# Performance work log

Hardware: AMD Instinct MI355X
Metric: run time of the kernel (lower is better)

## Reference

```python
import jax, jax.numpy as jnp
import numpy as np

DROPOUT_P = 0.5

def _gcn_conv(h, W, b, src, dst, norm, self_norm, n):
    # h: [N, Din] -> [N, Dout]; symmetric-normalized aggregation with self loops
    h = h @ W
    msg = h[src] * norm[:, None]                       # [E, Dout]
    agg = jax.ops.segment_sum(msg, dst, num_segments=n)
    return agg + h * self_norm[:, None] + b


def setup_inputs() -> dict:
    key = jax.random.key(0)
    ks = jax.random.split(key, 8)
    N, E, D_IN, D_OUT = 50000, 800000, 512, 256
    H = 2 * D_OUT  # 512
    x = jax.random.normal(ks[0], (N, D_IN), dtype=jnp.float32)
    edge_index = jax.random.randint(ks[1], (2, E), 0, N, dtype=jnp.int64)
    s = 1.0 / np.sqrt(D_IN)
    W1 = jax.random.uniform(ks[2], (D_IN, H), jnp.float32, -s, s)
    b1 = jnp.zeros((H,), jnp.float32)
    s2 = 1.0 / np.sqrt(H)
    Wmu = jax.random.uniform(ks[3], (H, D_OUT), jnp.float32, -s2, s2)
    bmu = jnp.zeros((D_OUT,), jnp.float32)
    Wls = jax.random.uniform(ks[4], (H, D_OUT), jnp.float32, -s2, s2)
    bls = jnp.zeros((D_OUT,), jnp.float32)
    return {"x": x, "edge_index": edge_index, "W1": W1, "b1": b1,
            "Wmu": Wmu, "bmu": bmu, "Wls": Wls, "bls": bls}


def reference(x, edge_index, W1, b1, Wmu, bmu, Wls, bls):
    n = x.shape[0]
    src, dst = edge_index[0], edge_index[1]
    # GCN symmetric normalization with self loops: deg includes +1 self loop
    deg = jax.ops.segment_sum(jnp.ones_like(dst, dtype=x.dtype), dst, num_segments=n) + 1.0
    dinv = jax.lax.rsqrt(deg)
    norm = dinv[src] * dinv[dst]     # per-edge norm
    self_norm = dinv * dinv          # self-loop norm = 1/deg
    # dropout (train mode, deterministic mask)
    keep = jax.random.bernoulli(jax.random.key(42), 1.0 - DROPOUT_P, x.shape)
    h = jnp.where(keep, x / (1.0 - DROPOUT_P), 0.0)
    h = jax.nn.relu(_gcn_conv(h, W1, b1, src, dst, norm, self_norm, n))
    mu = _gcn_conv(h, Wmu, bmu, src, dst, norm, self_norm, n)
    logstd = _gcn_conv(h, Wls, bls, src, dst, norm, self_norm, n)
    return (mu, logstd)
```

## Files before the change

### kernel.cpp

```cpp
#include <hip/hip_runtime.h>
#include <hip/hip_bf16.h>

typedef __hip_bfloat16 bf16;
typedef __attribute__((ext_vector_type(8))) short short8;
typedef __attribute__((ext_vector_type(4))) float f32x4;

__device__ __forceinline__ float bfu(unsigned short b) {
    unsigned u = ((unsigned)b) << 16;
    float f;
    __builtin_memcpy(&f, &u, 4);
    return f;
}
__device__ __forceinline__ unsigned short f2b(float f) {
    return (unsigned short)(__hip_bfloat16_raw(__float2bfloat16(f)).x);
}

__device__ __forceinline__ void gl_lds16(const void* g, void* l) {
    __builtin_amdgcn_global_load_lds(
        (const __attribute__((address_space(1))) void*)g,
        (__attribute__((address_space(3))) void*)l, 16, 0, 0);
}

__device__ __forceinline__ bool keep_elem(unsigned idx) {
    const unsigned k0 = 0u, k1 = 42u;
    const unsigned k2 = k0 ^ k1 ^ 0x1BD11BDAu;
    unsigned x0 = k0;
    unsigned x1 = idx + k1;
#define TF_QR(R) { x0 += x1; x1 = (x1 << R) | (x1 >> (32 - R)); x1 ^= x0; }
    TF_QR(13) TF_QR(15) TF_QR(26) TF_QR(6)
    x0 += k1; x1 += k2 + 1u;
    TF_QR(17) TF_QR(29) TF_QR(16) TF_QR(24)
    x0 += k2; x1 += k0 + 2u;
    TF_QR(13) TF_QR(15) TF_QR(26) TF_QR(6)
    x0 += k0; x1 += k1 + 3u;
    TF_QR(17) TF_QR(29) TF_QR(16) TF_QR(24)
    x0 += k1; x1 += k2 + 4u;
    TF_QR(13) TF_QR(15) TF_QR(26) TF_QR(6)
    x0 += k2; x1 += k0 + 5u;
#undef TF_QR
    return (((x0 ^ x1) >> 31) & 1u) == 0u;
}

__global__ void detect_edges_k(const unsigned* __restrict__ w, int* __restrict__ flag) {
    __shared__ unsigned red[256];
    unsigned v = 0;
    for (int i = threadIdx.x; i < 2048; i += 256) v |= w[2 * i + 1];
    red[threadIdx.x] = v;
    __syncthreads();
    for (int s = 128; s > 0; s >>= 1) {
        if (threadIdx.x < s) red[threadIdx.x] |= red[threadIdx.x + s];
        __syncthreads();
    }
    if (threadIdx.x == 0) flag[0] = (red[0] == 0u) ? 1 : 0;
}

__global__ void detect_f32_k(const unsigned short* __restrict__ w,
                             int* __restrict__ flag, int fidx) {
    __shared__ int red[256];
    int cnt = 0;
    for (int i = threadIdx.x; i < 1024; i += 256) {
        unsigned short b = w[2 * i];
        int e = (b >> 7) & 0xFF;
        if ((b & 0x7FFF) == 0 || (e >= 100 && e < 140)) cnt++;
    }
    red[threadIdx.x] = cnt;
    __syncthreads();
    for (int s = 128; s > 0; s >>= 1) {
        if (threadIdx.x < s) red[threadIdx.x] += red[threadIdx.x + s];
        __syncthreads();
    }
    if (threadIdx.x == 0) flag[fidx] = (red[0] < 614) ? 1 : 0;
}

__global__ void convert_edges_k(const void* __restrict__ src, int* __restrict__ out,
                                int twoE, const int* __restrict__ flag) {
    int i = blockIdx.x * 256 + threadIdx.x;
    if (i >= twoE) return;
    if (flag[0]) out[i] = (int)((const unsigned long long*)src)[i];
    else         out[i] = ((const int*)src)[i];
}

__global__ void canon_x_drop_k(const void* __restrict__ src, bf16* __restrict__ dst,
                               int n8, const int* __restrict__ flag) {
    int i = blockIdx.x * 256 + threadIdx.x;
    if (i >= n8) return;
    float v[8];
    if (flag[1]) {
        const f32x4* p = (const f32x4*)src;
        f32x4 a = p[2 * i], b = p[2 * i + 1];
#pragma unroll
        for (int k = 0; k < 4; ++k) { v[k] = a[k]; v[4 + k] = b[k]; }
    } else {
        short8 u = ((const short8*)src)[i];
#pragma unroll
        for (int k = 0; k < 8; ++k) v[k] = bfu((unsigned short)u[k]);
    }
    unsigned base = (unsigned)i * 8u;
    short8 o;
#pragma unroll
    for (int k = 0; k < 8; ++k) {
        float f = keep_elem(base + k) ? v[k] * 2.0f : 0.0f;
        o[k] = (short)f2b(f);
    }
    ((short8*)dst)[i] = o;
}

__global__ void canon_k(const void* __restrict__ src, bf16* __restrict__ dst,
                        int n, const int* __restrict__ flag, int fidx) {
    int i = blockIdx.x * 256 + threadIdx.x;
    if (i >= n) return;
    if (flag[fidx]) dst[i] = __float2bfloat16(((const float*)src)[i]);
    else            dst[i] = ((const bf16*)src)[i];
}

__global__ void canon_transpose_k(const void* __restrict__ src, unsigned short* __restrict__ dst,
                                  int K, int Nn, const int* __restrict__ flag, int fidx) {
    __shared__ unsigned short tile[16][17];
    int k0 = blockIdx.x * 16, n0 = blockIdx.y * 16;
    int k = k0 + threadIdx.y, n = n0 + threadIdx.x;
    unsigned short v;
    if (flag[fidx]) v = f2b(((const float*)src)[(size_t)k * Nn + n]);
    else            v = ((const unsigned short*)src)[(size_t)k * Nn + n];
    tile[threadIdx.y][threadIdx.x] = v;
    __syncthreads();
    int nn = n0 + threadIdx.y, kk = k0 + threadIdx.x;
    dst[(size_t)nn * K + kk] = tile[threadIdx.x][threadIdx.y];
}

__global__ void zero_int_k(int* __restrict__ p, int n) {
    int i = blockIdx.x * 256 + threadIdx.x;
    if (i < n) p[i] = 0;
}
__global__ void deg_count_k(const int* __restrict__ edges, int* __restrict__ degi,
                            int E, int n) {
    int e = blockIdx.x * 256 + threadIdx.x;
    if (e >= E) return;
    int d = edges[E + e];
    d = (d < 0) ? 0 : (d >= n ? n - 1 : d);
    atomicAdd(&degi[d], 1);
}
__global__ void dinv_k(const int* __restrict__ degi, float* __restrict__ dinv, int n) {
    int i = blockIdx.x * 256 + threadIdx.x;
    if (i < n) dinv[i] = rsqrtf(1.0f + (float)degi[i]);
}
__global__ void block_sums_k(const int* __restrict__ deg, int* __restrict__ partial, int n) {
    __shared__ int sh[256];
    int i = blockIdx.x * 256 + threadIdx.x;
    sh[threadIdx.x] = (i < n) ? deg[i] : 0;
    __syncthreads();
    for (int s = 128; s > 0; s >>= 1) {
        if (threadIdx.x < s) sh[threadIdx.x] += sh[threadIdx.x + s];
        __syncthreads();
    }
    if (threadIdx.x == 0) partial[blockIdx.x] = sh[0];
}
__global__ void scan_partials_k(int* __restrict__ partial, int G) {
    __shared__ int sh[256];
    int v = (threadIdx.x < G) ? partial[threadIdx.x] : 0;
    sh[threadIdx.x] = v;
    __syncthreads();
    for (int s = 1; s < 256; s <<= 1) {
        int t = 0;
        if (threadIdx.x >= s) t = sh[threadIdx.x - s];
        __syncthreads();
        sh[threadIdx.x] += t;
        __syncthreads();
    }
    if (threadIdx.x < G) partial[threadIdx.x] = sh[threadIdx.x] - v;
}
__global__ void scan_block_k(const int* __restrict__ deg, const int* __restrict__ partial,
                             int* __restrict__ row_ptr, int n) {
    __shared__ int sh[256];
    int i = blockIdx.x * 256 + threadIdx.x;
    int v = (i < n) ? deg[i] : 0;
    sh[threadIdx.x] = v;
    __syncthreads();
    for (int s = 1; s < 256; s <<= 1) {
        int t = 0;
        if (threadIdx.x >= s) t = sh[threadIdx.x - s];
        __syncthreads();
        sh[threadIdx.x] += t;
        __syncthreads();
    }
    int incl = sh[threadIdx.x];
    int base = partial[blockIdx.x];
    if (i < n) row_ptr[i] = base + incl - v;
    if (i == n - 1) row_ptr[n] = base + incl;
}
__global__ void fill_k(const int* __restrict__ edges, const int* __restrict__ row_ptr,
                       int* __restrict__ cnt, int* __restrict__ col, int E, int n) {
    int e = blockIdx.x * 256 + threadIdx.x;
    if (e >= E) return;
    int s = edges[e], d = edges[E + e];
    s = (s < 0) ? 0 : (s >= n ? n - 1 : s);
    d = (d < 0) ? 0 : (d >= n ? n - 1 : d);
    int pos = row_ptr[d] + atomicAdd(&cnt[d], 1);
    col[pos] = s;
}

__global__ __launch_bounds__(256) void gemm_mfma_k(
    const bf16* __restrict__ A, const bf16* __restrict__ Bt,
    bf16* __restrict__ Cb, float* __restrict__ Cf, float* __restrict__ Cf2,
    const bf16* __restrict__ bias, int M, int Nn, int K, int split) {
    __shared__ short sA[128 * 32];
    __shared__ short sB[128 * 32];
    const int tid = threadIdx.x;
    const int lane = tid & 63;
    const int w = tid >> 6;
    const int m0 = blockIdx.x * 128;
    const int n0 = blockIdx.y * 128;
    const int wm = (w >> 1) * 64;
    const int wn = (w & 1) * 64;

    f32x4 acc[4][4] = {};

    const int srow = lane >> 2;
    const int scol = (lane & 3) * 8;

    for (int kk = 0; kk < K; kk += 32) {
#pragma unroll
        for (int q = 0; q < 2; ++q) {
            int r = q * 64 + w * 16 + srow;
            int grow = m0 + r; if (grow >= M) grow = M - 1;
            gl_lds16(A + (size_t)grow * K + kk + scol, &sA[q * 2048 + w * 512 + lane * 8]);
        }
#pragma unroll
        for (int q = 0; q < 2; ++q) {
            int r = q * 64 + w * 16 + srow;
            gl_lds16(Bt + (size_t)(n0 + r) * K + kk + scol, &sB[q * 2048 + w * 512 + lane * 8]);
        }
        __syncthreads();

        const int fr = lane & 15;
        const int fk = (lane >> 4) * 8;
        short8 af[4], bfr[4];
#pragma unroll
        for (int i = 0; i < 4; ++i)
            af[i] = *(const short8*)&sA[(wm + i * 16 + fr) * 32 + fk];
#pragma unroll
        for (int j = 0; j < 4; ++j)
            bfr[j] = *(const short8*)&sB[(wn + j * 16 + fr) * 32 + fk];
#pragma unroll
        for (int i = 0; i < 4; ++i)
#pragma unroll
            for (int j = 0; j < 4; ++j)
                acc[i][j] = __builtin_amdgcn_mfma_f32_16x16x32_bf16(
                    af[i], bfr[j], acc[i][j], 0, 0, 0);
        __syncthreads();
    }

    const int crow = (lane >> 4) * 4;
    const int ccol = lane & 15;
    float* fbase = Cf;
    int nb = n0 + wn;
    int stride = Nn;
    if (Cf2) {
        stride = split;
        if (nb >= split) { fbase = Cf2; nb -= split; }
    }
#pragma unroll
    for (int i = 0; i < 4; ++i) {
#pragma unroll
        for (int r = 0; r < 4; ++r) {
            int row = m0 + wm + i * 16 + crow + r;
            if (row >= M) continue;
            if (Cf) {
                float* cp = fbase + (size_t)row * stride + nb;
#pragma unroll
                for (int j = 0; j < 4; ++j) {
                    int c = j * 16 + ccol;
                    cp[c] = acc[i][j][r] + __bfloat162float(bias[n0 + wn + c]);
                }
            } else {
                bf16* cp = Cb + (size_t)row * Nn + n0 + wn;
#pragma unroll
                for (int j = 0; j < 4; ++j)
                    cp[j * 16 + ccol] = __float2bfloat16(acc[i][j][r]);
            }
        }
    }
}

__global__ __launch_bounds__(256) void gather_k(
    const bf16* __restrict__ t, const int* __restrict__ row_ptr,
    const int* __restrict__ col, const float* __restrict__ dinv,
    const bf16* __restrict__ bias, bf16* __restrict__ outp, int mode, int N) {
    const int node = blockIdx.x * 4 + (threadIdx.x >> 6);
    if (node >= N) return;
    const int lane = threadIdx.x & 63;
    const short8* tp = (const short8*)t;
    const int beg = row_ptr[node];
    const int end = row_ptr[node + 1];
    const float dv = dinv[node];
    float acc[8] = {0.f, 0.f, 0.f, 0.f, 0.f, 0.f, 0.f, 0.f};

    int e = beg;
    const int elim = beg + ((end - beg) & ~7);
    if (e < elim) {
        int c[8];
        float w[8];
#pragma unroll
        for (int k = 0; k < 8; ++k) c[k] = col[e + k];
#pragma unroll
        for (int k = 0; k < 8; ++k) w[k] = dinv[c[k]] * dv;
        for (;;) {
            short8 u[8];
#pragma unroll
            for (int k = 0; k < 8; ++k) u[k] = tp[(size_t)c[k] * 64 + lane];
            const int en = e + 8;
            const bool more = en < elim;
            int cn[8];
            float wn2[8];
            if (more) {
#pragma unroll
                for (int k = 0; k < 8; ++k) cn[k] = col[en + k];
#pragma unroll
                for (int k = 0; k < 8; ++k) wn2[k] = dinv[cn[k]] * dv;
            }
#pragma unroll
            for (int k = 0; k < 8; ++k) {
                const float wk = w[k];
#pragma unroll
                for (int j = 0; j < 8; ++j)
                    acc[j] += wk * bfu((unsigned short)u[k][j]);
            }
            e = en;
            if (!more) break;
#pragma unroll
            for (int k = 0; k < 8; ++k) { c[k] = cn[k]; w[k] = wn2[k]; }
        }
    }
    for (; e + 4 <= end; e += 4) {
        int s0 = col[e + 0], s1 = col[e + 1], s2 = col[e + 2], s3 = col[e + 3];
        float w0 = dinv[s0] * dv, w1 = dinv[s1] * dv;
        float w2 = dinv[s2] * dv, w3 = dinv[s3] * dv;
        short8 u0 = tp[(size_t)s0 * 64 + lane];
        short8 u1 = tp[(size_t)s1 * 64 + lane];
        short8 u2 = tp[(size_t)s2 * 64 + lane];
        short8 u3 = tp[(size_t)s3 * 64 + lane];
#pragma unroll
        for (int k = 0; k < 8; ++k) {
            acc[k] += w0 * bfu((unsigned short)u0[k]);
            acc[k] += w1 * bfu((unsigned short)u1[k]);
            acc[k] += w2 * bfu((unsigned short)u2[k]);
            acc[k] += w3 * bfu((unsigned short)u3[k]);
        }
    }
    for (; e < end; ++e) {
        int s = col[e];
        float w = dinv[s] * dv;
        short8 u = tp[(size_t)s * 64 + lane];
#pragma unroll
        for (int k = 0; k < 8; ++k) acc[k] += w * bfu((unsigned short)u[k]);
    }
    {
        short8 u = tp[(size_t)node * 64 + lane];
        float w = dv * dv;
#pragma unroll
        for (int k = 0; k < 8; ++k) acc[k] += w * bfu((unsigned short)u[k]);
    }
    if (mode == 1) {
        short8 bs = ((const short8*)bias)[lane];
#pragma unroll
        for (int k = 0; k < 8; ++k) {
            acc[k] += bfu((unsigned short)bs[k]);
            acc[k] = fmaxf(acc[k], 0.f);
        }
    }
    short8 o;
#pragma unroll
    for (int k = 0; k < 8; ++k) o[k] = (short)f2b(acc[k]);
    ((short8*)outp)[(size_t)node * 64 + lane] = o;
}

extern "C" void kernel_launch(void* const* d_in, const int* in_sizes, int n_in,
                              void* d_out, int out_size, void* d_ws, size_t ws_size,
                              hipStream_t stream) {
    const void* xin   = d_in[0];
    const void* ei    = d_in[1];
    const void* W1in  = d_in[2];
    const void* b1in  = d_in[3];
    const void* Wmuin = d_in[4];
    const void* bmuin = d_in[5];
    const void* Wlsin = d_in[6];
    const void* blsin = d_in[7];
    float* out = (float*)d_out;

    const int H    = in_sizes[3];
    const int DOUT = in_sizes[5];
    const int DIN  = in_sizes[2] / H;
    const int N    = in_sizes[0] / DIN;
    const int E    = in_sizes[1] / 2;
    const int G    = (N + 255) / 256;

    char* ws = (char*)d_ws;
    size_t off = 0;
    auto alloc = [&](size_t bytes) {
        void* p = ws + off;
        off = (off + bytes + 255) & ~(size_t)255;
        return p;
    };
    int*   flag    = (int*)alloc(256);
    int*   edges   = (int*)alloc((size_t)2 * E * 4);
    int*   degi    = (int*)alloc((size_t)N * 4);
    int*   row_ptr = (int*)alloc((size_t)(N + 1) * 4);
    int*   cnt     = (int*)alloc((size_t)N * 4);
    int*   partial = (int*)alloc((size_t)G * 4);
    int*   col     = (int*)alloc((size_t)E * 4);
    float* dinv    = (float*)alloc((size_t)N * 4);
    bf16*  t1      = (bf16*)alloc((size_t)N * H * 2);
    bf16*  g1      = (bf16*)alloc((size_t)N * H * 2);
    bf16*  xdrop   = (bf16*)alloc((size_t)N * DIN * 2);
    bf16*  W1t     = (bf16*)alloc((size_t)DIN * H * 2);
    bf16*  Wcat    = (bf16*)alloc((size_t)H * 2 * DOUT * 2);
    bf16*  b1c     = (bf16*)alloc((size_t)H * 2);
    bf16*  bcat    = (bf16*)alloc((size_t)2 * DOUT * 2);
    if (off > ws_size) return;

    const int twoE = 2 * E;
    hipLaunchKernelGGL(detect_edges_k, dim3(1), dim3(256), 0, stream, (const unsigned*)ei, flag);
    hipLaunchKernelGGL(detect_f32_k, dim3(1), dim3(256), 0, stream, (const unsigned short*)xin, flag, 1);
    hipLaunchKernelGGL(detect_f32_k, dim3(1), dim3(256), 0, stream, (const unsigned short*)W1in, flag, 2);

    hipLaunchKernelGGL(convert_edges_k, dim3((twoE + 255) / 256), dim3(256), 0, stream,
                       ei, edges, twoE, flag);
    int n8 = (N * DIN) / 8;
    hipLaunchKernelGGL(canon_x_drop_k, dim3((n8 + 255) / 256), dim3(256), 0, stream,
                       xin, xdrop, n8, flag);
    hipLaunchKernelGGL(canon_transpose_k, dim3(DIN / 16, H / 16), dim3(16, 16), 0, stream,
                       W1in, (unsigned short*)W1t, DIN, H, flag, 2);
    hipLaunchKernelGGL(canon_transpose_k, dim3(H / 16, DOUT / 16), dim3(16, 16), 0, stream,
                       Wmuin, (unsigned short*)Wcat, H, DOUT, flag, 2);
    hipLaunchKernelGGL(canon_transpose_k, dim3(H / 16, DOUT / 16), dim3(16, 16), 0, stream,
                       Wlsin, (unsigned short*)(Wcat + (size_t)DOUT * H), H, DOUT, flag, 2);
    hipLaunchKernelGGL(canon_k, dim3(2), dim3(256), 0, stream, b1in, b1c, H, flag, 2);
    hipLaunchKernelGGL(canon_k, dim3(1), dim3(256), 0, stream, bmuin, bcat, DOUT, flag, 2);
    hipLaunchKernelGGL(canon_k, dim3(1), dim3(256), 0, stream, blsin, bcat + DOUT, DOUT, flag, 2);

    hipLaunchKernelGGL(zero_int_k, dim3(G), dim3(256), 0, stream, degi, N);
    hipLaunchKernelGGL(zero_int_k, dim3(G), dim3(256), 0, stream, cnt, N);
    hipLaunchKernelGGL(deg_count_k, dim3((E + 255) / 256), dim3(256), 0, stream, edges, degi, E, N);
    hipLaunchKernelGGL(dinv_k, dim3(G), dim3(256), 0, stream, degi, dinv, N);
    hipLaunchKernelGGL(block_sums_k, dim3(G), dim3(256), 0, stream, degi, partial, N);
    hipLaunchKernelGGL(scan_partials_k, dim3(1), dim3(256), 0, stream, partial, G);
    hipLaunchKernelGGL(scan_block_k, dim3(G), dim3(256), 0, stream, degi, partial, row_ptr, N);
    hipLaunchKernelGGL(fill_k, dim3((E + 255) / 256), dim3(256), 0, stream, edges, row_ptr, cnt, col, E, N);

    hipLaunchKernelGGL(gemm_mfma_k, dim3((N + 127) / 128, H / 128), dim3(256), 0, stream,
                       xdrop, W1t, t1, (float*)nullptr, (float*)nullptr,
                       (const bf16*)nullptr, N, H, DIN, 0);
    bf16* h1 = xdrop;
    hipLaunchKernelGGL(gather_k, dim3((N + 3) / 4), dim3(256), 0, stream,
                       t1, row_ptr, col, dinv, b1c, h1, 1, N);

    hipLaunchKernelGGL(gather_k, dim3((N + 3) / 4), dim3(256), 0, stream,
                       h1, row_ptr, col, dinv, (const bf16*)nullptr, g1, 0, N);
    hipLaunchKernelGGL(gemm_mfma_k, dim3((N + 127) / 128, (2 * DOUT) / 128), dim3(256), 0, stream,
                       g1, Wcat, (bf16*)nullptr, out, out + (size_t)N * DOUT,
                       bcat, N, 2 * DOUT, H, DOUT);
}
```

Before: 659.1 us.

## Fuse dropout into GEMM A-load, widen GEMM tile to full N, merge small kernels

The dropout-and-convert pass over x moves inside the first GEMM's A-tile load, so the bf16 xdrop buffer is never written and read back. The GEMM becomes a 512-thread kernel that covers all 512 output columns per 128-row block, so each A tile is loaded once instead of four times. Flag detection, bias conversion, counter zeroing and dinv are merged into fewer launches. In exchange the Philox-style mask is recomputed in the GEMM's load path with no double buffering, LDS use grows, and occupancy may drop.

```diff
diff --git a/kernel.cpp b/kernel.cpp
--- a/kernel.cpp
+++ b/kernel.cpp
@@ -41,35 +41,37 @@
     return (((x0 ^ x1) >> 31) & 1u) == 0u;
 }
 
-__global__ void detect_edges_k(const unsigned* __restrict__ w, int* __restrict__ flag) {
-    __shared__ unsigned red[256];
-    unsigned v = 0;
-    for (int i = threadIdx.x; i < 2048; i += 256) v |= w[2 * i + 1];
-    red[threadIdx.x] = v;
-    __syncthreads();
-    for (int s = 128; s > 0; s >>= 1) {
-        if (threadIdx.x < s) red[threadIdx.x] |= red[threadIdx.x + s];
-        __syncthreads();
-    }
-    if (threadIdx.x == 0) flag[0] = (red[0] == 0u) ? 1 : 0;
-}
-
-__global__ void detect_f32_k(const unsigned short* __restrict__ w,
-                             int* __restrict__ flag, int fidx) {
+__global__ void detect_all_k(const unsigned* __restrict__ ei,
+                             const unsigned short* __restrict__ x,
+                             const unsigned short* __restrict__ w1,
+                             int* __restrict__ flag) {
     __shared__ int red[256];
-    int cnt = 0;
-    for (int i = threadIdx.x; i < 1024; i += 256) {
-        unsigned short b = w[2 * i];
-        int e = (b >> 7) & 0xFF;
-        if ((b & 0x7FFF) == 0 || (e >= 100 && e < 140)) cnt++;
-    }
-    red[threadIdx.x] = cnt;
-    __syncthreads();
-    for (int s = 128; s > 0; s >>= 1) {
-        if (threadIdx.x < s) red[threadIdx.x] += red[threadIdx.x + s];
-        __syncthreads();
-    }
-    if (threadIdx.x == 0) flag[fidx] = (red[0] < 614) ? 1 : 0;
+    if (blockIdx.x == 0) {
+        unsigned v = 0;
+        for (int i = threadIdx.x; i < 2048; i += 256) v |= ei[2 * i + 1];
+        red[threadIdx.x] = (int)v;
+        __syncthreads();
+        for (int s = 128; s > 0; s >>= 1) {
+            if (threadIdx.x < s) red[threadIdx.x] |= red[threadIdx.x + s];
+            __syncthreads();
+        }
+        if (threadIdx.x == 0) flag[0] = (red[0] == 0) ? 1 : 0;
+    } else {
+        const unsigned short* p = (blockIdx.x == 1) ? x : w1;
+        int cnt = 0;
+        for (int i = threadIdx.x; i < 1024; i += 256) {
+            unsigned short b = p[2 * i];
+            int e = (b >> 7) & 0xFF;
+            if ((b & 0x7FFF) == 0 || (e >= 100 && e < 140)) cnt++;
+        }
+        red[threadIdx.x] = cnt;
+        __syncthreads();
+        for (int s = 128; s > 0; s >>= 1) {
+            if (threadIdx.x < s) red[threadIdx.x] += red[threadIdx.x + s];
+            __syncthreads();
+        }
+        if (threadIdx.x == 0) flag[blockIdx.x] = (red[0] < 614) ? 1 : 0;
+    }
 }
 
 __global__ void convert_edges_k(const void* __restrict__ src, int* __restrict__ out,
@@ -78,39 +80,6 @@
     if (i >= twoE) return;
     if (flag[0]) out[i] = (int)((const unsigned long long*)src)[i];
     else         out[i] = ((const int*)src)[i];
-}
-
-__global__ void canon_x_drop_k(const void* __restrict__ src, bf16* __restrict__ dst,
-                               int n8, const int* __restrict__ flag) {
-    int i = blockIdx.x * 256 + threadIdx.x;
-    if (i >= n8) return;
-    float v[8];
-    if (flag[1]) {
-        const f32x4* p = (const f32x4*)src;
-        f32x4 a = p[2 * i], b = p[2 * i + 1];
-#pragma unroll
-        for (int k = 0; k < 4; ++k) { v[k] = a[k]; v[4 + k] = b[k]; }
-    } else {
-        short8 u = ((const short8*)src)[i];
-#pragma unroll
-        for (int k = 0; k < 8; ++k) v[k] = bfu((unsigned short)u[k]);
-    }
-    unsigned base = (unsigned)i * 8u;
-    short8 o;
-#pragma unroll
-    for (int k = 0; k < 8; ++k) {
-        float f = keep_elem(base + k) ? v[k] * 2.0f : 0.0f;
-        o[k] = (short)f2b(f);
-    }
-    ((short8*)dst)[i] = o;
-}
-
-__global__ void canon_k(const void* __restrict__ src, bf16* __restrict__ dst,
-                        int n, const int* __restrict__ flag, int fidx) {
-    int i = blockIdx.x * 256 + threadIdx.x;
-    if (i >= n) return;
-    if (flag[fidx]) dst[i] = __float2bfloat16(((const float*)src)[i]);
-    else            dst[i] = ((const bf16*)src)[i];
 }
 
 __global__ void canon_transpose_k(const void* __restrict__ src, unsigned short* __restrict__ dst,
@@ -127,6 +96,23 @@
     dst[(size_t)nn * K + kk] = tile[threadIdx.x][threadIdx.y];
 }
 
+__global__ void canon_bias_k(const void* __restrict__ b1, const void* __restrict__ bmu,
+                             const void* __restrict__ bls, bf16* __restrict__ b1c,
+                             bf16* __restrict__ bcat, int H, int DOUT,
+                             const int* __restrict__ flag) {
+    int i = blockIdx.x * 256 + threadIdx.x;
+    int f = flag[2];
+    if (i < H) {
+        b1c[i] = f ? __float2bfloat16(((const float*)b1)[i]) : ((const bf16*)b1)[i];
+    } else if (i < H + DOUT) {
+        int j = i - H;
+        bcat[j] = f ? __float2bfloat16(((const float*)bmu)[j]) : ((const bf16*)bmu)[j];
+    } else if (i < H + 2 * DOUT) {
+        int j = i - H - DOUT;
+        bcat[DOUT + j] = f ? __float2bfloat16(((const float*)bls)[j]) : ((const bf16*)bls)[j];
+    }
+}
+
 __global__ void zero_int_k(int* __restrict__ p, int n) {
     int i = blockIdx.x * 256 + threadIdx.x;
     if (i < n) p[i] = 0;
@@ -138,10 +124,6 @@
     int d = edges[E + e];
     d = (d < 0) ? 0 : (d >= n ? n - 1 : d);
     atomicAdd(&degi[d], 1);
-}
-__global__ void dinv_k(const int* __restrict__ degi, float* __restrict__ dinv, int n) {
-    int i = blockIdx.x * 256 + threadIdx.x;
-    if (i < n) dinv[i] = rsqrtf(1.0f + (float)degi[i]);
 }
 __global__ void block_sums_k(const int* __restrict__ deg, int* __restrict__ partial, int n) {
     __shared__ int sh[256];
@@ -169,7 +151,7 @@
     if (threadIdx.x < G) partial[threadIdx.x] = sh[threadIdx.x] - v;
 }
 __global__ void scan_block_k(const int* __restrict__ deg, const int* __restrict__ partial,
-                             int* __restrict__ row_ptr, int n) {
+                             int* __restrict__ row_ptr, float* __restrict__ dinv, int n) {
     __shared__ int sh[256];
     int i = blockIdx.x * 256 + threadIdx.x;
     int v = (i < n) ? deg[i] : 0;
@@ -184,7 +166,10 @@
     }
     int incl = sh[threadIdx.x];
     int base = partial[blockIdx.x];
-    if (i < n) row_ptr[i] = base + incl - v;
+    if (i < n) {
+        row_ptr[i] = base + incl - v;
+        dinv[i] = rsqrtf(1.0f + (float)v);
+    }
     if (i == n - 1) row_ptr[n] = base + incl;
 }
 __global__ void fill_k(const int* __restrict__ edges, const int* __restrict__ row_ptr,
@@ -198,83 +183,106 @@
     col[pos] = s;
 }
 
-__global__ __launch_bounds__(256) void gemm_mfma_k(
-    const bf16* __restrict__ A, const bf16* __restrict__ Bt,
+__global__ __launch_bounds__(512) void gemm_wide_k(
+    const void* __restrict__ Ain, const bf16* __restrict__ Bt,
     bf16* __restrict__ Cb, float* __restrict__ Cf, float* __restrict__ Cf2,
-    const bf16* __restrict__ bias, int M, int Nn, int K, int split) {
+    const bf16* __restrict__ bias, int M, int K,
+    const int* __restrict__ flag, int drop) {
     __shared__ short sA[128 * 32];
-    __shared__ short sB[128 * 32];
+    __shared__ short sB[512 * 32];
     const int tid = threadIdx.x;
     const int lane = tid & 63;
     const int w = tid >> 6;
     const int m0 = blockIdx.x * 128;
-    const int n0 = blockIdx.y * 128;
-    const int wm = (w >> 1) * 64;
-    const int wn = (w & 1) * 64;
-
-    f32x4 acc[4][4] = {};
-
-    const int srow = lane >> 2;
-    const int scol = (lane & 3) * 8;
+    const int wm = (w & 1) * 64;
+    const int wn = (w >> 1) * 128;
+
+    f32x4 acc[4][8] = {};
+
+    const int arow = tid >> 2;
+    const int acol = (tid & 3) * 8;
+    int grow = m0 + arow;
+    if (grow >= M) grow = M - 1;
+    const bool xf32 = drop && flag[1];
 
     for (int kk = 0; kk < K; kk += 32) {
 #pragma unroll
-        for (int q = 0; q < 2; ++q) {
-            int r = q * 64 + w * 16 + srow;
-            int grow = m0 + r; if (grow >= M) grow = M - 1;
-            gl_lds16(A + (size_t)grow * K + kk + scol, &sA[q * 2048 + w * 512 + lane * 8]);
-        }
-#pragma unroll
-        for (int q = 0; q < 2; ++q) {
-            int r = q * 64 + w * 16 + srow;
-            gl_lds16(Bt + (size_t)(n0 + r) * K + kk + scol, &sB[q * 2048 + w * 512 + lane * 8]);
+        for (int q = 0; q < 4; ++q)
+            gl_lds16(Bt + (size_t)(q * 128 + arow) * K + kk + acol,
+                     &sB[q * 4096 + tid * 8]);
+        if (!drop) {
+            gl_lds16((const bf16*)Ain + (size_t)grow * K + kk + acol, &sA[tid * 8]);
+        } else {
+            unsigned gidx = (unsigned)grow * (unsigned)K + (unsigned)(kk + acol);
+            float v[8];
+            if (xf32) {
+                const f32x4* p = (const f32x4*)Ain;
+                f32x4 a = p[gidx >> 2], b = p[(gidx >> 2) + 1];
+#pragma unroll
+                for (int k2 = 0; k2 < 4; ++k2) { v[k2] = a[k2]; v[4 + k2] = b[k2]; }
+            } else {
+                short8 u = ((const short8*)Ain)[gidx >> 3];
+#pragma unroll
+                for (int k2 = 0; k2 < 8; ++k2) v[k2] = bfu((unsigned short)u[k2]);
+            }
+            short8 o;
+#pragma unroll
+            for (int k2 = 0; k2 < 8; ++k2) {
+                float f = keep_elem(gidx + k2) ? v[k2] * 2.0f : 0.0f;
+                o[k2] = (short)f2b(f);
+            }
+            *(short8*)&sA[tid * 8] = o;
         }
         __syncthreads();
 
         const int fr = lane & 15;
         const int fk = (lane >> 4) * 8;
-        short8 af[4], bfr[4];
+        short8 af[4], bfr2[8];
 #pragma unroll
         for (int i = 0; i < 4; ++i)
             af[i] = *(const short8*)&sA[(wm + i * 16 + fr) * 32 + fk];
 #pragma unroll
-        for (int j = 0; j < 4; ++j)
-            bfr[j] = *(const short8*)&sB[(wn + j * 16 + fr) * 32 + fk];
+        for (int j = 0; j < 8; ++j)
+            bfr2[j] = *(const short8*)&sB[(wn + j * 16 + fr) * 32 + fk];
 #pragma unroll
         for (int i = 0; i < 4; ++i)
 #pragma unroll
-            for (int j = 0; j < 4; ++j)
+            for (int j = 0; j < 8; ++j)
                 acc[i][j] = __builtin_amdgcn_mfma_f32_16x16x32_bf16(
-                    af[i], bfr[j], acc[i][j], 0, 0, 0);
+                    af[i], bfr2[j], acc[i][j], 0, 0, 0);
         __syncthreads();
     }
 
     const int crow = (lane >> 4) * 4;
     const int ccol = lane & 15;
-    float* fbase = Cf;
-    int nb = n0 + wn;
-    int stride = Nn;
-    if (Cf2) {
-        stride = split;
-        if (nb >= split) { fbase = Cf2; nb -= split; }
-    }
-#pragma unroll
-    for (int i = 0; i < 4; ++i) {
-#pragma unroll
-        for (int r = 0; r < 4; ++r) {
-            int row = m0 + wm + i * 16 + crow + r;
-            if (row >= M) continue;
-            if (Cf) {
-                float* cp = fbase + (size_t)row * stride + nb;
-#pragma unroll
-                for (int j = 0; j < 4; ++j) {
+    if (Cf) {
+        const int side = (wn >= 256) ? 1 : 0;
+        float* base = side ? Cf2 : Cf;
+        const int nb = wn - side * 256;
+#pragma unroll
+        for (int i = 0; i < 4; ++i) {
+#pragma unroll
+            for (int r = 0; r < 4; ++r) {
+                int row = m0 + wm + i * 16 + crow + r;
+                if (row >= M) continue;
+                float* cp = base + (size_t)row * 256 + nb;
+#pragma unroll
+                for (int j = 0; j < 8; ++j) {
                     int c = j * 16 + ccol;
-                    cp[c] = acc[i][j][r] + __bfloat162float(bias[n0 + wn + c]);
+                    cp[c] = acc[i][j][r] + __bfloat162float(bias[wn + c]);
                 }
-            } else {
-                bf16* cp = Cb + (size_t)row * Nn + n0 + wn;
-#pragma unroll
-                for (int j = 0; j < 4; ++j)
+            }
+        }
+    } else {
+#pragma unroll
+        for (int i = 0; i < 4; ++i) {
+#pragma unroll
+            for (int r = 0; r < 4; ++r) {
+                int row = m0 + wm + i * 16 + crow + r;
+                if (row >= M) continue;
+                bf16* cp = Cb + (size_t)row * 512 + wn;
+#pragma unroll
+                for (int j = 0; j < 8; ++j)
                     cp[j * 16 + ccol] = __float2bfloat16(acc[i][j][r]);
             }
         }
@@ -402,15 +410,16 @@
     };
     int*   flag    = (int*)alloc(256);
     int*   edges   = (int*)alloc((size_t)2 * E * 4);
-    int*   degi    = (int*)alloc((size_t)N * 4);
+    int*   degcnt  = (int*)alloc((size_t)2 * N * 4);
+    int*   degi    = degcnt;
+    int*   cnt     = degcnt + N;
     int*   row_ptr = (int*)alloc((size_t)(N + 1) * 4);
-    int*   cnt     = (int*)alloc((size_t)N * 4);
     int*   partial = (int*)alloc((size_t)G * 4);
     int*   col     = (int*)alloc((size_t)E * 4);
     float* dinv    = (float*)alloc((size_t)N * 4);
     bf16*  t1      = (bf16*)alloc((size_t)N * H * 2);
     bf16*  g1      = (bf16*)alloc((size_t)N * H * 2);
-    bf16*  xdrop   = (bf16*)alloc((size_t)N * DIN * 2);
+    bf16*  h1      = (bf16*)alloc((size_t)N * H * 2);
     bf16*  W1t     = (bf16*)alloc((size_t)DIN * H * 2);
     bf16*  Wcat    = (bf16*)alloc((size_t)H * 2 * DOUT * 2);
     bf16*  b1c     = (bf16*)alloc((size_t)H * 2);
@@ -418,44 +427,37 @@
     if (off > ws_size) return;
 
     const int twoE = 2 * E;
-    hipLaunchKernelGGL(detect_edges_k, dim3(1), dim3(256), 0, stream, (const unsigned*)ei, flag);
-    hipLaunchKernelGGL(detect_f32_k, dim3(1), dim3(256), 0, stream, (const unsigned short*)xin, flag, 1);
-    hipLaunchKernelGGL(detect_f32_k, dim3(1), dim3(256), 0, stream, (const unsigned short*)W1in, flag, 2);
+    hipLaunchKernelGGL(detect_all_k, dim3(3), dim3(256), 0, stream,
+                       (const unsigned*)ei, (const unsigned short*)xin,
+                       (const unsigned short*)W1in, flag);
 
     hipLaunchKernelGGL(convert_edges_k, dim3((twoE + 255) / 256), dim3(256), 0, stream,
                        ei, edges, twoE, flag);
-    int n8 = (N * DIN) / 8;
-    hipLaunchKernelGGL(canon_x_drop_k, dim3((n8 + 255) / 256), dim3(256), 0, stream,
-                       xin, xdrop, n8, flag);
     hipLaunchKernelGGL(canon_transpose_k, dim3(DIN / 16, H / 16), dim3(16, 16), 0, stream,
                        W1in, (unsigned short*)W1t, DIN, H, flag, 2);
     hipLaunchKernelGGL(canon_transpose_k, dim3(H / 16, DOUT / 16), dim3(16, 16), 0, stream,
                        Wmuin, (unsigned short*)Wcat, H, DOUT, flag, 2);
     hipLaunchKernelGGL(canon_transpose_k, dim3(H / 16, DOUT / 16), dim3(16, 16), 0, stream,
                        Wlsin, (unsigned short*)(Wcat + (size_t)DOUT * H), H, DOUT, flag, 2);
-    hipLaunchKernelGGL(canon_k, dim3(2), dim3(256), 0, stream, b1in, b1c, H, flag, 2);
-    hipLaunchKernelGGL(canon_k, dim3(1), dim3(256), 0, stream, bmuin, bcat, DOUT, flag, 2);
-    hipLaunchKernelGGL(canon_k, dim3(1), dim3(256), 0, stream, blsin, bcat + DOUT, DOUT, flag, 2);
-
-    hipLaunchKernelGGL(zero_int_k, dim3(G), dim3(256), 0, stream, degi, N);
-    hipLaunchKernelGGL(zero_int_k, dim3(G), dim3(256), 0, stream, cnt, N);
+    hipLaunchKernelGGL(canon_bias_k, dim3((H + 2 * DOUT + 255) / 256), dim3(256), 0, stream,
+                       b1in, bmuin, blsin, b1c, bcat, H, DOUT, flag);
+
+    hipLaunchKernelGGL(zero_int_k, dim3((2 * N + 255) / 256), dim3(256), 0, stream, degcnt, 2 * N);
     hipLaunchKernelGGL(deg_count_k, dim3((E + 255) / 256), dim3(256), 0, stream, edges, degi, E, N);
-    hipLaunchKernelGGL(dinv_k, dim3(G), dim3(256), 0, stream, degi, dinv, N);
     hipLaunchKernelGGL(block_sums_k, dim3(G), dim3(256), 0, stream, degi, partial, N);
     hipLaunchKernelGGL(scan_partials_k, dim3(1), dim3(256), 0, stream, partial, G);
-    hipLaunchKernelGGL(scan_block_k, dim3(G), dim3(256), 0, stream, degi, partial, row_ptr, N);
+    hipLaunchKernelGGL(scan_block_k, dim3(G), dim3(256), 0, stream, degi, partial, row_ptr, dinv, N);
     hipLaunchKernelGGL(fill_k, dim3((E + 255) / 256), dim3(256), 0, stream, edges, row_ptr, cnt, col, E, N);
 
-    hipLaunchKernelGGL(gemm_mfma_k, dim3((N + 127) / 128, H / 128), dim3(256), 0, stream,
-                       xdrop, W1t, t1, (float*)nullptr, (float*)nullptr,
-                       (const bf16*)nullptr, N, H, DIN, 0);
-    bf16* h1 = xdrop;
+    hipLaunchKernelGGL(gemm_wide_k, dim3((N + 127) / 128), dim3(512), 0, stream,
+                       xin, W1t, t1, (float*)nullptr, (float*)nullptr,
+                       (const bf16*)nullptr, N, DIN, flag, 1);
     hipLaunchKernelGGL(gather_k, dim3((N + 3) / 4), dim3(256), 0, stream,
                        t1, row_ptr, col, dinv, b1c, h1, 1, N);
 
     hipLaunchKernelGGL(gather_k, dim3((N + 3) / 4), dim3(256), 0, stream,
                        h1, row_ptr, col, dinv, (const bf16*)nullptr, g1, 0, N);
-    hipLaunchKernelGGL(gemm_mfma_k, dim3((N + 127) / 128, (2 * DOUT) / 128), dim3(256), 0, stream,
+    hipLaunchKernelGGL(gemm_wide_k, dim3((N + 127) / 128), dim3(512), 0, stream,
                        g1, Wcat, (bf16*)nullptr, out, out + (size_t)N * DOUT,
-                       bcat, N, 2 * DOUT, H, DOUT);
-}
+                       bcat, N, H, flag, 0);
+}
```

After: 668.2 us. No clear change (+1.4%).
